# Performance work log

Measured on AMD Instinct MI355X. Metric: run time of the kernel, lower is better.

## Reference

```python
import jax, jax.numpy as jnp
import numpy as np

WIDE = 15
PAD = (WIDE - 1) // 2
FREQS = np.array([1., 2., 3., 4., 5., 6.], dtype=np.float32)  # wave_base_ml frequencies


def _lstm_dir(x, wih, whh, b):
    # x: [B,T,F]; wih: [4H,F]; whh: [4H,H]; b: [4H] (b_ih+b_hh fused)
    H = whh.shape[1]
    xg = jnp.einsum('btf,gf->btg', x, wih) + b  # precompute input projections
    def step(carry, xt):
        h, c = carry
        g = xt + h @ whh.T
        i, f, gg, o = jnp.split(g, 4, axis=-1)  # torch gate order i,f,g,o
        c = jax.nn.sigmoid(f) * c + jax.nn.sigmoid(i) * jnp.tanh(gg)
        h = jax.nn.sigmoid(o) * jnp.tanh(c)
        return (h, c), h
    h0 = jnp.zeros((x.shape[0], H), x.dtype)
    _, hs = jax.lax.scan(step, (h0, h0), jnp.swapaxes(xg, 0, 1))
    return jnp.swapaxes(hs, 0, 1)


def _bn(x, g, b, eps=1e-5):
    # training-mode BatchNorm1d over (N, L) per channel; x: [B,C,L]
    m = jnp.mean(x, axis=(0, 2), keepdims=True)
    v = jnp.var(x, axis=(0, 2), keepdims=True)
    return (x - m) * jax.lax.rsqrt(v + eps) * g[None, :, None] + b[None, :, None]


def _conv1d(x, w, b):
    y = jax.lax.conv_general_dilated(x, w, (1,), 'VALID', dimension_numbers=('NCH', 'OIH', 'NCH'))
    return y + b[None, :, None]


def _haar(x):
    s = 0.7071067811865476
    return (x[..., ::2] + x[..., 1::2]) * s, (x[..., ::2] - x[..., 1::2]) * s


def _forward(x, lstm_wif, lstm_whf, lstm_bf, lstm_wir, lstm_whr, lstm_br, base_w, base_b,
             g1, be1, g2, be2, g3, be3, g4, be4, g5, be5,
             w2, b2, w3, b3, w4, b4, w5, b5, fcw, fcb):
    xt = jnp.swapaxes(x, 1, 2)  # [B,T,F]
    fwd = _lstm_dir(xt, lstm_wif, lstm_whf, lstm_bf)
    bwd = _lstm_dir(xt[:, ::-1], lstm_wir, lstm_whr, lstm_br)[:, ::-1]
    X = jnp.swapaxes(jnp.concatenate([fwd, bwd], axis=-1), 1, 2)  # [B,C,T], C=2*dim
    B, C, T = X.shape
    Xp = jnp.pad(X, ((0, 0), (0, 0), (PAD, PAD)))
    # shared sliding windows [B,C,T,WIDE] used both for scale conv and Furi_conv
    Xwin = jnp.stack([Xp[..., k:k + T] for k in range(WIDE)], axis=-1)
    offs = (jnp.arange(WIDE, dtype=X.dtype) - PAD) / WIDE
    outs = []
    for ii in range(len(FREQS)):
        scales = jax.nn.relu(jnp.einsum('bctk,k->bct', Xwin, base_w[ii]) + base_b[ii])
        # per-position cosine Fourier basis generated from the learned scales
        bases = jnp.cos((2.0 * np.pi * FREQS[ii]) * scales[..., None] * offs)  # [B,C,T,WIDE]
        o = jnp.sum(Xwin * bases, axis=-1)  # position-dependent (dynamic) conv
        sqrs = jnp.sqrt((jnp.trunc(scales * WIDE) + 1.0) / (WIDE + 2) * 2.0)
        outs.append(o / sqrs)
    wave = jnp.stack(outs, axis=1).reshape(B, -1, T)  # [B, n_waves*C, T] (wave-major, matches torch cat+view)
    out = _bn(wave, g1, be1)
    out = _bn(jax.nn.relu(_conv1d(out, w2, b2)), g2, be2)
    out = _bn(jax.nn.relu(_conv1d(out, w3, b3)), g3, be3)
    out_back = out  # [B, V_dim, L3]
    out = _bn(jax.nn.relu(_conv1d(out, w4, b4)), g4, be4)  # [B,16,L3-2]
    # 4-level Haar DWT; 5 subbands upsampled to L3, averaged over channels
    a1, d1 = _haar(out_back); a2, d2 = _haar(a1); a3, d3 = _haar(a2); a4, d4 = _haar(a3)
    L3 = out_back.shape[-1]
    bands = [jnp.repeat(bb, L3 // bb.shape[-1], axis=-1) for bb in (a4, d4, d3, d2, d1)]
    dwt = jnp.stack([bb.mean(axis=1) for bb in bands], axis=1)  # [B,5,L3]
    odwt = _bn(jax.nn.relu(_conv1d(dwt, w5, b5)), g5, be5)  # [B,16,L3-2]
    out = jnp.concatenate([out, odwt], axis=-1)
    out = out.mean(axis=-1)  # AdaptiveAvgPool1d(1) + squeeze
    return out @ fcw.T + fcb


def setup_inputs() -> dict:
    key = jax.random.key(0)
    ks = iter(jax.random.split(key, 40))
    def p(shape, s=0.05):
        return jax.random.normal(next(ks), shape, jnp.float32) * s
    B, F, T, DIM, NW, Vd = 32, 64, 518, 64, 6, 32
    C = 2 * DIM
    return {
        'x': jax.random.normal(next(ks), (B, F, T), jnp.float32),
        'lstm_wif': p((4 * DIM, F)), 'lstm_whf': p((4 * DIM, DIM)), 'lstm_bf': p((4 * DIM,)),
        'lstm_wir': p((4 * DIM, F)), 'lstm_whr': p((4 * DIM, DIM)), 'lstm_br': p((4 * DIM,)),
        'base_w': p((NW, WIDE)), 'base_b': p((NW,)),
        'g1': jnp.ones((C * NW,)), 'be1': jnp.zeros((C * NW,)),
        'g2': jnp.ones((128,)), 'be2': jnp.zeros((128,)),
        'g3': jnp.ones((Vd,)), 'be3': jnp.zeros((Vd,)),
        'g4': jnp.ones((16,)), 'be4': jnp.zeros((16,)),
        'g5': jnp.ones((16,)), 'be5': jnp.zeros((16,)),
        'w2': p((128, C * NW, 3)), 'b2': p((128,)),
        'w3': p((Vd, 128, 5)), 'b3': p((Vd,)),
        'w4': p((16, Vd, 3)), 'b4': p((16,)),
        'w5': p((16, 5, 3)), 'b5': p((16,)),
        'fcw': p((10, 16)), 'fcb': p((10,)),
    }


def reference(x, lstm_wif, lstm_whf, lstm_bf, lstm_wir, lstm_whr, lstm_br, base_w, base_b,
              g1, be1, g2, be2, g3, be3, g4, be4, g5, be5,
              w2, b2, w3, b3, w4, b4, w5, b5, fcw, fcb):
    return _forward(x, lstm_wif, lstm_whf, lstm_bf, lstm_wir, lstm_whr, lstm_br, base_w, base_b,
                    g1, be1, g2, be2, g3, be3, g4, be4, g5, be5,
                    w2, b2, w3, b3, w4, b4, w5, b5, fcw, fcb)
```

## Files before the change

### kernel.cpp

```cpp
#include <hip/hip_runtime.h>
#include <math.h>

#define B_     32
#define F_     64
#define T_     518
#define HID    64
#define GATES  256
#define CCH    128
#define NWAVE  6
#define WCH    768
#define L2_    516
#define L3_    512
#define L4_    510

__device__ __forceinline__ float frcp(float x) { return __builtin_amdgcn_rcpf(x); }
__device__ __forceinline__ float fsigmoid(float x) { return frcp(1.f + __expf(-x)); }
__device__ __forceinline__ float ftanh(float x) { return 1.f - 2.f * frcp(1.f + __expf(2.f * x)); }

#define PIN8(a0,a1,a2,a3,a4,a5,a6,a7) \
    asm volatile("" : "+v"(a0), "+v"(a1), "+v"(a2), "+v"(a3), \
                      "+v"(a4), "+v"(a5), "+v"(a6), "+v"(a7))

__global__ void xg_kernel(const float* __restrict__ x,
                          const float* __restrict__ wif, const float* __restrict__ bf,
                          const float* __restrict__ wir, const float* __restrict__ br,
                          float* __restrict__ xg_f, float* __restrict__ xg_r,
                          float* __restrict__ stats) {
    if (blockIdx.x == 0 && blockIdx.y == 0) {
        for (int i = threadIdx.x; i < 2 * WCH; i += 256) stats[i] = 0.f;
    }
    const int tid = threadIdx.x;
    const int g   = tid;
    const int b   = blockIdx.y;
    const int t0  = blockIdx.x * 8;
    float4 wa[16], wb[16];
    const float4* w0 = (const float4*)(wif + g * F_);
    const float4* w1 = (const float4*)(wir + g * F_);
#pragma unroll
    for (int i = 0; i < 16; ++i) { wa[i] = w0[i]; wb[i] = w1[i]; }
    const float bfv = bf[g], brv = br[g];
    for (int tt = 0; tt < 8; ++tt) {
        const int t = t0 + tt;
        if (t >= T_) break;
        const float* xp = x + (size_t)b * F_ * T_ + t;
        float a0 = bfv, a1 = brv;
#pragma unroll
        for (int i = 0; i < 16; ++i) {
            float x0 = xp[(i * 4 + 0) * T_];
            float x1 = xp[(i * 4 + 1) * T_];
            float x2 = xp[(i * 4 + 2) * T_];
            float x3 = xp[(i * 4 + 3) * T_];
            a0 += wa[i].x * x0 + wa[i].y * x1 + wa[i].z * x2 + wa[i].w * x3;
            a1 += wb[i].x * x0 + wb[i].y * x1 + wb[i].z * x2 + wb[i].w * x3;
        }
        const size_t o = ((size_t)b * T_ + t) * GATES + tid;
        xg_f[o] = a0;
        xg_r[o] = a1;
    }
}

__global__ __attribute__((amdgpu_flat_work_group_size(256, 256),
                          amdgpu_waves_per_eu(1, 1)))
void lstm_kernel(
        const float* __restrict__ xgi_f, const float* __restrict__ xgi_r,
        const float* __restrict__ whf, const float* __restrict__ whr,
        float* __restrict__ X) {
    const int dir = blockIdx.x & 1;
    const int b   = blockIdx.x >> 1;
    const float* xg  = (dir ? xgi_r : xgi_f) + (size_t)b * T_ * GATES;
    const float* whh = dir ? whr : whf;
    const int tid = threadIdx.x;
    const int r   = tid & 63;
    const int w   = tid >> 6;

    float wreg[64];
    {
        const float4* p = (const float4*)(whh + (size_t)(w * HID + r) * HID);
#pragma unroll
        for (int i = 0; i < 16; ++i) {
            const float4 v = p[i];
            wreg[4 * i] = v.x; wreg[4 * i + 1] = v.y;
            wreg[4 * i + 2] = v.z; wreg[4 * i + 3] = v.w;
        }
    }
#pragma unroll
    for (int i = 0; i < 64; i += 8)
        PIN8(wreg[i], wreg[i + 1], wreg[i + 2], wreg[i + 3],
             wreg[i + 4], wreg[i + 5], wreg[i + 6], wreg[i + 7]);

    __shared__ __align__(16) float hs[4][HID];
    __shared__ float gbuf[2][4][HID];
    hs[w][r] = 0.f;
    float c = 0.f;
    float* Xrow = X + ((size_t)(b * CCH + dir * HID + r)) * T_;

    int t = dir ? (T_ - 1) : 0;
    const int step = dir ? -1 : 1;
    float q0 = xg[(size_t)t * GATES + tid];
    float q1 = xg[(size_t)(t + step) * GATES + tid];

    for (int s = 0; s < T_; ++s) {
        float a0 = q0, a1 = 0.f, a2 = 0.f, a3 = 0.f;
        const float4* h4p = (const float4*)hs[w];
#pragma unroll
        for (int i = 0; i < 16; ++i) {
            const float4 h4 = h4p[i];
            a0 = fmaf(wreg[4 * i], h4.x, a0);
            a1 = fmaf(wreg[4 * i + 1], h4.y, a1);
            a2 = fmaf(wreg[4 * i + 2], h4.z, a2);
            a3 = fmaf(wreg[4 * i + 3], h4.w, a3);
        }
        const int buf = s & 1;
        gbuf[buf][w][r] = (a0 + a1) + (a2 + a3);

        int tp = t + 2 * step;
        tp = tp < 0 ? 0 : (tp >= T_ ? T_ - 1 : tp);
        const float qn = xg[(size_t)tp * GATES + tid];

        asm volatile("s_waitcnt lgkmcnt(0)" ::: "memory");
        __builtin_amdgcn_s_barrier();

        const float gi = gbuf[buf][0][r];
        const float gf = gbuf[buf][1][r];
        const float gg = gbuf[buf][2][r];
        const float go = gbuf[buf][3][r];
        const float si = fsigmoid(gi);
        const float sf = fsigmoid(gf);
        const float so = fsigmoid(go);
        c = sf * c + si * ftanh(gg);
        const float h = so * ftanh(c);

        hs[w][r] = h;
        if (w == 0) Xrow[t] = h;
        q0 = q1; q1 = qn;
        t += step;
    }
}

__global__ void wave_kernel(const float* __restrict__ X,
                            const float* __restrict__ bw, const float* __restrict__ bb,
                            float* __restrict__ wave, float* __restrict__ stats) {
    const int b = blockIdx.z, c = blockIdx.y;
    const int t0 = blockIdx.x * 256;
    const int tid = threadIdx.x;
    __shared__ float xs[256 + 14];
    __shared__ float bws[NWAVE][16];
    __shared__ float bbs[NWAVE];
    __shared__ float red[4][12];
    const float* xrow = X + ((size_t)(b * CCH + c)) * T_;
    for (int i = tid; i < 270; i += 256) {
        int tt = t0 - 7 + i;
        xs[i] = (tt >= 0 && tt < T_) ? xrow[tt] : 0.f;
    }
    if (tid < NWAVE * 15) bws[tid / 15][tid % 15] = bw[tid];
    if (tid < NWAVE) bbs[tid] = bb[tid];
    __syncthreads();
    const int t = t0 + tid;
    float ls[NWAVE], lq[NWAVE];
#pragma unroll
    for (int ii = 0; ii < NWAVE; ++ii) { ls[ii] = 0.f; lq[ii] = 0.f; }
    if (t < T_) {
        float win[15];
#pragma unroll
        for (int k = 0; k < 15; ++k) win[k] = xs[tid + k];
        float e[8];
        e[0] = win[7];
#pragma unroll
        for (int m = 1; m < 8; ++m) e[m] = win[7 - m] + win[7 + m];
        const float c0 = 6.28318530717958647692f / 15.f;
#pragma unroll
        for (int ii = 0; ii < NWAVE; ++ii) {
            float sc = bbs[ii];
#pragma unroll
            for (int k = 0; k < 15; ++k) sc += win[k] * bws[ii][k];
            sc = fmaxf(sc, 0.f);
            const float phi = c0 * (float)(ii + 1) * sc;
            float o = e[0];
#pragma unroll
            for (int m = 1; m < 8; ++m) o += e[m] * __cosf(phi * (float)m);
            const float q = (truncf(sc * 15.f) + 1.f) * (2.f / 17.f);
            const float val = o * rsqrtf(q);
            wave[((size_t)(b * WCH + ii * CCH + c)) * T_ + t] = val;
            ls[ii] = val;
            lq[ii] = val * val;
        }
    }
#pragma unroll
    for (int off = 32; off > 0; off >>= 1) {
#pragma unroll
        for (int ii = 0; ii < NWAVE; ++ii) {
            ls[ii] += __shfl_down(ls[ii], off);
            lq[ii] += __shfl_down(lq[ii], off);
        }
    }
    if ((tid & 63) == 0) {
        const int w = tid >> 6;
#pragma unroll
        for (int ii = 0; ii < NWAVE; ++ii) { red[w][ii] = ls[ii]; red[w][6 + ii] = lq[ii]; }
    }
    __syncthreads();
    if (tid < 12) {
        const float a = red[0][tid] + red[1][tid] + red[2][tid] + red[3][tid];
        const int ii = tid % 6;
        const int ch = ii * CCH + c;
        atomicAdd(&stats[(tid >= 6 ? WCH : 0) + ch], a);
    }
}

__global__ void bn1_finalize_kernel(const float* __restrict__ stats,
                                    float* __restrict__ mean, float* __restrict__ rstd) {
    const int c = threadIdx.x;
    const float n = (float)(B_ * T_);
    const float m = stats[c] / n;
    const float v = stats[WCH + c] / n - m * m;
    mean[c] = m;
    rstd[c] = rsqrtf(v + 1e-5f);
}

__global__ void bn_stats_kernel(const float* __restrict__ x, int Bn, int C, int L,
                                float* __restrict__ mean, float* __restrict__ rstd) {
    const int c = blockIdx.x;
    const int tid = threadIdx.x;
    float s = 0.f, s2 = 0.f;
    for (int b = 0; b < Bn; ++b) {
        const float* row = x + ((size_t)b * C + c) * L;
        for (int l = tid; l < L; l += 256) { float v = row[l]; s += v; s2 += v * v; }
    }
#pragma unroll
    for (int off = 32; off > 0; off >>= 1) { s += __shfl_down(s, off); s2 += __shfl_down(s2, off); }
    __shared__ float ss[4], ss2[4];
    if ((tid & 63) == 0) { ss[tid >> 6] = s; ss2[tid >> 6] = s2; }
    __syncthreads();
    if (tid == 0) {
        float S = ss[0] + ss[1] + ss[2] + ss[3];
        float S2 = ss2[0] + ss2[1] + ss2[2] + ss2[3];
        float n = (float)(Bn * L);
        float m = S / n;
        float v = S2 / n - m * m;
        mean[c] = m;
        rstd[c] = rsqrtf(v + 1e-5f);
    }
}

__global__ void bnfold2_kernel(const float* __restrict__ w2, const float* __restrict__ b2,
                               const float* __restrict__ m1, const float* __restrict__ r1,
                               const float* __restrict__ g1, const float* __restrict__ be1,
                               float* __restrict__ w2t, float* __restrict__ b2t) {
    const int o = blockIdx.x, tid = threadIdx.x;
    float part = 0.f;
    for (int idx = tid; idx < WCH * 3; idx += 256) {
        const int c = idx / 3;
        const float sc = r1[c] * g1[c];
        const float sh = be1[c] - m1[c] * sc;
        const float wv = w2[(size_t)o * (WCH * 3) + idx];
        w2t[(size_t)idx * 128 + o] = wv * sc;
        part += wv * sh;
    }
#pragma unroll
    for (int off = 32; off > 0; off >>= 1) part += __shfl_down(part, off);
    __shared__ float red[4];
    if ((tid & 63) == 0) red[tid >> 6] = part;
    __syncthreads();
    if (tid == 0) b2t[o] = b2[o] + red[0] + red[1] + red[2] + red[3];
}

__global__ void bnfold3_kernel(const float* __restrict__ w3, const float* __restrict__ b3,
                               const float* __restrict__ m2, const float* __restrict__ r2,
                               const float* __restrict__ g2, const float* __restrict__ be2,
                               float* __restrict__ w3t, float* __restrict__ b3t) {
    const int o = blockIdx.x, tid = threadIdx.x;
    float part = 0.f;
    for (int idx = tid; idx < 128 * 5; idx += 256) {
        const int c = idx / 5;
        const float sc = r2[c] * g2[c];
        const float sh = be2[c] - m2[c] * sc;
        const float wv = w3[(size_t)o * 640 + idx];
        w3t[(size_t)idx * 32 + o] = wv * sc;
        part += wv * sh;
    }
#pragma unroll
    for (int off = 32; off > 0; off >>= 1) part += __shfl_down(part, off);
    __shared__ float red[4];
    if ((tid & 63) == 0) red[tid >> 6] = part;
    __syncthreads();
    if (tid == 0) b3t[o] = b3[o] + red[0] + red[1] + red[2] + red[3];
}

__global__ void bnfold4_kernel(const float* __restrict__ w4, const float* __restrict__ b4,
                               const float* __restrict__ m3, const float* __restrict__ r3,
                               const float* __restrict__ g3, const float* __restrict__ be3,
                               float* __restrict__ w4t, float* __restrict__ b4t,
                               float* __restrict__ bnp3) {
    const int o = blockIdx.x, tid = threadIdx.x;
    float part = 0.f;
    if (tid < 96) {
        const int c = tid / 3;
        const float sc = r3[c] * g3[c];
        const float sh = be3[c] - m3[c] * sc;
        const float wv = w4[(size_t)o * 96 + tid];
        w4t[(size_t)tid * 16 + o] = wv * sc;
        part = wv * sh;
    }
    if (o == 0 && tid >= 96) {
        const int ch = tid - 96;
        const float sc = r3[ch] * g3[ch];
        bnp3[ch] = sc;
        bnp3[32 + ch] = be3[ch] - m3[ch] * sc;
    }
#pragma unroll
    for (int off = 32; off > 0; off >>= 1) part += __shfl_down(part, off);
    __shared__ float red[2];
    if ((tid & 63) == 0) red[tid >> 6] = part;
    __syncthreads();
    if (tid == 0) b4t[o] = b4[o] + red[0] + red[1];
}

__global__ __launch_bounds__(256) void conv2_kernel(
        const float* __restrict__ in, const float* __restrict__ wt,
        const float* __restrict__ bt, float* __restrict__ out) {
    const int b  = blockIdx.x;
    const int t  = blockIdx.y * 256 + threadIdx.x;
    const int o0 = blockIdx.z * 16;
    if (t >= L2_) return;
    float acc[16];
#pragma unroll
    for (int j = 0; j < 16; ++j) acc[j] = bt[o0 + j];
    const float* inb = in + (size_t)b * WCH * T_ + t;
    for (int c = 0; c < WCH; ++c) {
        const float x0 = inb[c * T_], x1 = inb[c * T_ + 1], x2 = inb[c * T_ + 2];
        const float* wc = wt + (size_t)c * 384 + o0;
#pragma unroll
        for (int j = 0; j < 16; ++j)
            acc[j] = fmaf(x0, wc[j], fmaf(x1, wc[128 + j], fmaf(x2, wc[256 + j], acc[j])));
    }
    const size_t ob = ((size_t)b * 128 + o0) * L2_ + t;
#pragma unroll
    for (int j = 0; j < 16; ++j) out[ob + (size_t)j * L2_] = fmaxf(acc[j], 0.f);
}

__global__ __launch_bounds__(256) void conv3_kernel(
        const float* __restrict__ in, const float* __restrict__ wt,
        const float* __restrict__ bt, float* __restrict__ out) {
    const int b  = blockIdx.x;
    const int t  = blockIdx.y * 256 + threadIdx.x;
    const int o0 = blockIdx.z * 8;
    float acc[8];
#pragma unroll
    for (int j = 0; j < 8; ++j) acc[j] = bt[o0 + j];
    const float* inb = in + (size_t)b * 128 * L2_ + t;
    for (int c = 0; c < 128; ++c) {
        const float x0 = inb[c * L2_], x1 = inb[c * L2_ + 1], x2 = inb[c * L2_ + 2];
        const float x3 = inb[c * L2_ + 3], x4 = inb[c * L2_ + 4];
        const float* wc = wt + (size_t)c * 160 + o0;
#pragma unroll
        for (int j = 0; j < 8; ++j) {
            float a = fmaf(x0, wc[j], acc[j]);
            a = fmaf(x1, wc[32 + j], a);
            a = fmaf(x2, wc[64 + j], a);
            a = fmaf(x3, wc[96 + j], a);
            acc[j] = fmaf(x4, wc[128 + j], a);
        }
    }
    const size_t ob = ((size_t)b * 32 + o0) * L3_ + t;
#pragma unroll
    for (int j = 0; j < 8; ++j) out[ob + (size_t)j * L3_] = fmaxf(acc[j], 0.f);
}

__global__ __launch_bounds__(256) void conv4_kernel(
        const float* __restrict__ in, const float* __restrict__ wt,
        const float* __restrict__ bt, float* __restrict__ out) {
    const int b = blockIdx.x;
    const int t = blockIdx.y * 256 + threadIdx.x;
    if (t >= L4_) return;
    float acc[16];
#pragma unroll
    for (int j = 0; j < 16; ++j) acc[j] = bt[j];
    const float* inb = in + (size_t)b * 32 * L3_ + t;
    for (int c = 0; c < 32; ++c) {
        const float x0 = inb[c * L3_], x1 = inb[c * L3_ + 1], x2 = inb[c * L3_ + 2];
        const float* wc = wt + (size_t)c * 48;
#pragma unroll
        for (int j = 0; j < 16; ++j)
            acc[j] = fmaf(x0, wc[j], fmaf(x1, wc[16 + j], fmaf(x2, wc[32 + j], acc[j])));
    }
    const size_t ob = ((size_t)b * 16) * L4_ + t;
#pragma unroll
    for (int j = 0; j < 16; ++j) out[ob + (size_t)j * L4_] = fmaxf(acc[j], 0.f);
}

__global__ __launch_bounds__(512) void dwt_conv5_kernel(const float* __restrict__ y3,
                                                        const float* __restrict__ w5,
                                                        const float* __restrict__ b5,
                                                        const float* __restrict__ bnp3,
                                                        float* __restrict__ y5) {
    const int b = blockIdx.x, l = threadIdx.x;
    __shared__ float cm[L3_];
    __shared__ float bands[5][L3_];
    __shared__ float w5s[240];
    __shared__ float b5s[16];
    __shared__ float sc3s[32], sh3s[32];
    if (l < 240) w5s[l] = w5[l];
    if (l < 16) b5s[l] = b5[l];
    if (l >= 256 && l < 288) sc3s[l - 256] = bnp3[l - 256];
    if (l >= 288 && l < 320) sh3s[l - 288] = bnp3[32 + (l - 288)];
    __syncthreads();
    float s = 0.f, shs = 0.f;
    for (int ch = 0; ch < 32; ++ch) {
        s = fmaf(y3[((size_t)b * 32 + ch) * L3_ + l], sc3s[ch], s);
        shs += sh3s[ch];
    }
    cm[l] = (s + shs) * (1.f / 32.f);
    __syncthreads();
    const float s1 = 0.70710678118654752440f;
    const float s2c = 0.5f;
    const float s3 = 0.35355339059327378f;
    const float s4 = 0.25f;
    const int b16 = l & ~15, b8 = l & ~7, b4v = l & ~3, b2v = l & ~1;
    float sa = 0.f, sb = 0.f;
#pragma unroll
    for (int i = 0; i < 8; ++i) { sa += cm[b16 + i]; sb += cm[b16 + 8 + i]; }
    bands[0][l] = (sa + sb) * s4;
    bands[1][l] = (sa - sb) * s4;
    float ta = 0.f, tb = 0.f;
#pragma unroll
    for (int i = 0; i < 4; ++i) { ta += cm[b8 + i]; tb += cm[b8 + 4 + i]; }
    bands[2][l] = (ta - tb) * s3;
    bands[3][l] = (cm[b4v] + cm[b4v + 1] - cm[b4v + 2] - cm[b4v + 3]) * s2c;
    bands[4][l] = (cm[b2v] - cm[b2v + 1]) * s1;
    __syncthreads();
    if (l < L4_) {
        float in3[5][3];
#pragma unroll
        for (int c = 0; c < 5; ++c) {
            in3[c][0] = bands[c][l]; in3[c][1] = bands[c][l + 1]; in3[c][2] = bands[c][l + 2];
        }
#pragma unroll
        for (int o = 0; o < 16; ++o) {
            float acc = b5s[o];
#pragma unroll
            for (int c = 0; c < 5; ++c) {
                const float* wp = &w5s[(o * 5 + c) * 3];
                acc += in3[c][0] * wp[0] + in3[c][1] * wp[1] + in3[c][2] * wp[2];
            }
            y5[((size_t)b * 16 + o) * L4_ + l] = fmaxf(acc, 0.f);
        }
    }
}

__global__ __launch_bounds__(512) void tail_final_kernel(
        const float* __restrict__ y4, const float* __restrict__ y5,
        const float* __restrict__ g4, const float* __restrict__ be4,
        const float* __restrict__ g5, const float* __restrict__ be5,
        const float* __restrict__ fcw, const float* __restrict__ fcb,
        float* __restrict__ out) {
    const int p = threadIdx.x;
    const int b = p >> 4, ch = p & 15;
    const float2* p4 = (const float2*)(y4 + ((size_t)(b * 16 + ch)) * L4_);
    const float2* p5 = (const float2*)(y5 + ((size_t)(b * 16 + ch)) * L4_);
    float s4 = 0.f, q4 = 0.f, s5 = 0.f, q5 = 0.f;
    for (int i = 0; i < L4_ / 2; ++i) {
        float2 a = p4[i], bb2 = p5[i];
        s4 += a.x + a.y;  q4 += a.x * a.x + a.y * a.y;
        s5 += bb2.x + bb2.y; q5 += bb2.x * bb2.x + bb2.y * bb2.y;
    }
    __shared__ float S4[512], Q4[512], S5[512], Q5[512];
    __shared__ float M4[16], R4[16], M5[16], R5[16];
    __shared__ float pool[B_][16];
    S4[p] = s4; Q4[p] = q4; S5[p] = s5; Q5[p] = q5;
    __syncthreads();
    if (p < 16) {
        float ts = 0.f, tq = 0.f, us = 0.f, uq = 0.f;
        for (int bb = 0; bb < B_; ++bb) {
            ts += S4[bb * 16 + p]; tq += Q4[bb * 16 + p];
            us += S5[bb * 16 + p]; uq += Q5[bb * 16 + p];
        }
        const float n = (float)(B_ * L4_);
        float m = ts / n; M4[p] = m; R4[p] = rsqrtf(tq / n - m * m + 1e-5f);
        m = us / n;       M5[p] = m; R5[p] = rsqrtf(uq / n - m * m + 1e-5f);
    }
    __syncthreads();
    {
        const float mm4 = s4 / (float)L4_, mm5 = s5 / (float)L4_;
        const float v4 = (mm4 - M4[ch]) * R4[ch] * g4[ch] + be4[ch];
        const float v5 = (mm5 - M5[ch]) * R5[ch] * g5[ch] + be5[ch];
        pool[b][ch] = 0.5f * (v4 + v5);
    }
    __syncthreads();
    if (p < B_ * 10) {
        const int bb = p / 10, row = p - bb * 10;
        float a = fcb[row];
#pragma unroll
        for (int c = 0; c < 16; ++c) a += pool[bb][c] * fcw[row * 16 + c];
        out[bb * 10 + row] = a;
    }
}

extern "C" void kernel_launch(void* const* d_in, const int* in_sizes, int n_in,
                              void* d_out, int out_size, void* d_ws, size_t ws_size,
                              hipStream_t stream) {
    (void)in_sizes; (void)n_in; (void)out_size; (void)ws_size;
    const float* x   = (const float*)d_in[0];
    const float* wif = (const float*)d_in[1];
    const float* whf = (const float*)d_in[2];
    const float* bf  = (const float*)d_in[3];
    const float* wir = (const float*)d_in[4];
    const float* whr = (const float*)d_in[5];
    const float* br  = (const float*)d_in[6];
    const float* bw  = (const float*)d_in[7];
    const float* bb  = (const float*)d_in[8];
    const float* g1  = (const float*)d_in[9];  const float* be1 = (const float*)d_in[10];
    const float* g2  = (const float*)d_in[11]; const float* be2 = (const float*)d_in[12];
    const float* g3  = (const float*)d_in[13]; const float* be3 = (const float*)d_in[14];
    const float* g4  = (const float*)d_in[15]; const float* be4 = (const float*)d_in[16];
    const float* g5  = (const float*)d_in[17]; const float* be5 = (const float*)d_in[18];
    const float* w2  = (const float*)d_in[19]; const float* b2  = (const float*)d_in[20];
    const float* w3  = (const float*)d_in[21]; const float* b3  = (const float*)d_in[22];
    const float* w4  = (const float*)d_in[23]; const float* b4  = (const float*)d_in[24];
    const float* w5  = (const float*)d_in[25]; const float* b5  = (const float*)d_in[26];
    const float* fcw = (const float*)d_in[27]; const float* fcb = (const float*)d_in[28];
    float* out = (float*)d_out;
    float* ws  = (float*)d_ws;

    float* xg_f  = ws;
    float* xg_r  = ws + 4243456;
    float* wave  = ws;
    float* X     = ws + 12730368;
    float* y2    = ws + 14852096;
    float* y3    = ws + 16965632;
    float* y4    = ws + 17489920;
    float* y5    = ws + 17751040;
    float* stats = ws + 18012160;
    float* m1 = ws + 18013696; float* r1 = m1 + 768;
    float* m2 = r1 + 768;      float* r2 = m2 + 128;
    float* m3 = r2 + 128;      float* r3 = m3 + 32;
    float* w2t  = X;
    float* b2t  = X + 294912;
    float* w3t  = X + 295040;
    float* b3t  = X + 315520;
    float* w4t  = X + 315552;
    float* b4t  = X + 317088;
    float* bnp3 = X + 317104;

    xg_kernel<<<dim3(65, 32), 256, 0, stream>>>(x, wif, bf, wir, br, xg_f, xg_r, stats);
    lstm_kernel<<<dim3(64), 256, 0, stream>>>(xg_f, xg_r, whf, whr, X);
    wave_kernel<<<dim3(3, CCH, B_), 256, 0, stream>>>(X, bw, bb, wave, stats);
    bn1_finalize_kernel<<<dim3(1), 768, 0, stream>>>(stats, m1, r1);
    bnfold2_kernel<<<dim3(128), 256, 0, stream>>>(w2, b2, m1, r1, g1, be1, w2t, b2t);
    conv2_kernel<<<dim3(32, 3, 8), 256, 0, stream>>>(wave, w2t, b2t, y2);
    bn_stats_kernel<<<dim3(128), 256, 0, stream>>>(y2, B_, 128, L2_, m2, r2);
    bnfold3_kernel<<<dim3(32), 256, 0, stream>>>(w3, b3, m2, r2, g2, be2, w3t, b3t);
    conv3_kernel<<<dim3(32, 2, 4), 256, 0, stream>>>(y2, w3t, b3t, y3);
    bn_stats_kernel<<<dim3(32), 256, 0, stream>>>(y3, B_, 32, L3_, m3, r3);
    bnfold4_kernel<<<dim3(16), 128, 0, stream>>>(w4, b4, m3, r3, g3, be3, w4t, b4t, bnp3);
    conv4_kernel<<<dim3(32, 2), 256, 0, stream>>>(y3, w4t, b4t, y4);
    dwt_conv5_kernel<<<dim3(B_), 512, 0, stream>>>(y3, w5, b5, bnp3, y5);
    tail_final_kernel<<<dim3(1), 512, 0, stream>>>(y4, y5, g4, be4, g5, be5, fcw, fcb, out);
}
```

Before: 1.066 ms.

## Halve LSTM block to two gates per thread and fuse BN stats into convs

The LSTM recurrence now runs with 128 threads per block. Each thread holds two gate rows of the recurrent weights in registers and reads an interleaved float2 gate input, which the xg kernel now writes in that interleaved order. This cuts the per-step wave count and barrier cost but doubles the FMA chain per thread and raises register pressure. Separately, the standalone BN stats and finalize kernels are removed: conv2 and conv3 accumulate per-channel sum and sum-of-squares with wave shuffles and atomics, and the bnfold kernels derive scale and shift from those sums in shared memory. This drops several launches and full re-reads of y2 and y3, at the cost of atomics and a less numerically robust variance formula.

```diff
diff --git a/kernel.cpp b/kernel.cpp
--- a/kernel.cpp
+++ b/kernel.cpp
@@ -30,7 +30,10 @@
         for (int i = threadIdx.x; i < 2 * WCH; i += 256) stats[i] = 0.f;
     }
     const int tid = threadIdx.x;
-    const int g   = tid;
+    const int wv  = tid >> 7;
+    const int g2  = tid & 1;
+    const int r   = (tid >> 1) & 63;
+    const int g   = (2 * wv + g2) * 64 + r;
     const int b   = blockIdx.y;
     const int t0  = blockIdx.x * 8;
     float4 wa[16], wb[16];
@@ -59,7 +62,7 @@
     }
 }
 
-__global__ __attribute__((amdgpu_flat_work_group_size(256, 256),
+__global__ __attribute__((amdgpu_flat_work_group_size(128, 128),
                           amdgpu_waves_per_eu(1, 1)))
 void lstm_kernel(
         const float* __restrict__ xgi_f, const float* __restrict__ xgi_r,
@@ -73,22 +76,26 @@
     const int r   = tid & 63;
     const int w   = tid >> 6;
 
-    float wreg[64];
+    float wrA[64], wrB[64];
     {
-        const float4* p = (const float4*)(whh + (size_t)(w * HID + r) * HID);
+        const float4* pA = (const float4*)(whh + (size_t)((2 * w) * HID + r) * HID);
+        const float4* pB = (const float4*)(whh + (size_t)((2 * w + 1) * HID + r) * HID);
 #pragma unroll
         for (int i = 0; i < 16; ++i) {
-            const float4 v = p[i];
-            wreg[4 * i] = v.x; wreg[4 * i + 1] = v.y;
-            wreg[4 * i + 2] = v.z; wreg[4 * i + 3] = v.w;
-        }
-    }
-#pragma unroll
-    for (int i = 0; i < 64; i += 8)
-        PIN8(wreg[i], wreg[i + 1], wreg[i + 2], wreg[i + 3],
-             wreg[i + 4], wreg[i + 5], wreg[i + 6], wreg[i + 7]);
-
-    __shared__ __align__(16) float hs[4][HID];
+            const float4 va = pA[i], vb = pB[i];
+            wrA[4 * i] = va.x; wrA[4 * i + 1] = va.y; wrA[4 * i + 2] = va.z; wrA[4 * i + 3] = va.w;
+            wrB[4 * i] = vb.x; wrB[4 * i + 1] = vb.y; wrB[4 * i + 2] = vb.z; wrB[4 * i + 3] = vb.w;
+        }
+    }
+#pragma unroll
+    for (int i = 0; i < 64; i += 8) {
+        PIN8(wrA[i], wrA[i + 1], wrA[i + 2], wrA[i + 3],
+             wrA[i + 4], wrA[i + 5], wrA[i + 6], wrA[i + 7]);
+        PIN8(wrB[i], wrB[i + 1], wrB[i + 2], wrB[i + 3],
+             wrB[i + 4], wrB[i + 5], wrB[i + 6], wrB[i + 7]);
+    }
+
+    __shared__ __align__(16) float hs[2][HID];
     __shared__ float gbuf[2][4][HID];
     hs[w][r] = 0.f;
     float c = 0.f;
@@ -96,26 +103,33 @@
 
     int t = dir ? (T_ - 1) : 0;
     const int step = dir ? -1 : 1;
-    float q0 = xg[(size_t)t * GATES + tid];
-    float q1 = xg[(size_t)(t + step) * GATES + tid];
+    const float2* xg2 = (const float2*)xg;
+    float2 q0 = xg2[(size_t)t * 128 + w * 64 + r];
+    float2 q1 = xg2[(size_t)(t + step) * 128 + w * 64 + r];
 
     for (int s = 0; s < T_; ++s) {
-        float a0 = q0, a1 = 0.f, a2 = 0.f, a3 = 0.f;
+        float a0 = q0.x, a1 = 0.f, a2 = 0.f, a3 = 0.f;
+        float b0 = q0.y, b1 = 0.f, b2 = 0.f, b3 = 0.f;
         const float4* h4p = (const float4*)hs[w];
 #pragma unroll
         for (int i = 0; i < 16; ++i) {
             const float4 h4 = h4p[i];
-            a0 = fmaf(wreg[4 * i], h4.x, a0);
-            a1 = fmaf(wreg[4 * i + 1], h4.y, a1);
-            a2 = fmaf(wreg[4 * i + 2], h4.z, a2);
-            a3 = fmaf(wreg[4 * i + 3], h4.w, a3);
+            a0 = fmaf(wrA[4 * i], h4.x, a0);
+            a1 = fmaf(wrA[4 * i + 1], h4.y, a1);
+            a2 = fmaf(wrA[4 * i + 2], h4.z, a2);
+            a3 = fmaf(wrA[4 * i + 3], h4.w, a3);
+            b0 = fmaf(wrB[4 * i], h4.x, b0);
+            b1 = fmaf(wrB[4 * i + 1], h4.y, b1);
+            b2 = fmaf(wrB[4 * i + 2], h4.z, b2);
+            b3 = fmaf(wrB[4 * i + 3], h4.w, b3);
         }
         const int buf = s & 1;
-        gbuf[buf][w][r] = (a0 + a1) + (a2 + a3);
+        gbuf[buf][2 * w][r]     = (a0 + a1) + (a2 + a3);
+        gbuf[buf][2 * w + 1][r] = (b0 + b1) + (b2 + b3);
 
         int tp = t + 2 * step;
         tp = tp < 0 ? 0 : (tp >= T_ ? T_ - 1 : tp);
-        const float qn = xg[(size_t)tp * GATES + tid];
+        const float2 qn = xg2[(size_t)tp * 128 + w * 64 + r];
 
         asm volatile("s_waitcnt lgkmcnt(0)" ::: "memory");
         __builtin_amdgcn_s_barrier();
@@ -207,54 +221,29 @@
     }
 }
 
-__global__ void bn1_finalize_kernel(const float* __restrict__ stats,
-                                    float* __restrict__ mean, float* __restrict__ rstd) {
-    const int c = threadIdx.x;
+__global__ void bnfold2_kernel(const float* __restrict__ w2, const float* __restrict__ b2,
+                               const float* __restrict__ stats1,
+                               const float* __restrict__ g1, const float* __restrict__ be1,
+                               float* __restrict__ w2t, float* __restrict__ b2t,
+                               float* __restrict__ stats2) {
+    const int o = blockIdx.x, tid = threadIdx.x;
+    __shared__ float scs[WCH], shs[WCH];
     const float n = (float)(B_ * T_);
-    const float m = stats[c] / n;
-    const float v = stats[WCH + c] / n - m * m;
-    mean[c] = m;
-    rstd[c] = rsqrtf(v + 1e-5f);
-}
-
-__global__ void bn_stats_kernel(const float* __restrict__ x, int Bn, int C, int L,
-                                float* __restrict__ mean, float* __restrict__ rstd) {
-    const int c = blockIdx.x;
-    const int tid = threadIdx.x;
-    float s = 0.f, s2 = 0.f;
-    for (int b = 0; b < Bn; ++b) {
-        const float* row = x + ((size_t)b * C + c) * L;
-        for (int l = tid; l < L; l += 256) { float v = row[l]; s += v; s2 += v * v; }
-    }
-#pragma unroll
-    for (int off = 32; off > 0; off >>= 1) { s += __shfl_down(s, off); s2 += __shfl_down(s2, off); }
-    __shared__ float ss[4], ss2[4];
-    if ((tid & 63) == 0) { ss[tid >> 6] = s; ss2[tid >> 6] = s2; }
-    __syncthreads();
-    if (tid == 0) {
-        float S = ss[0] + ss[1] + ss[2] + ss[3];
-        float S2 = ss2[0] + ss2[1] + ss2[2] + ss2[3];
-        float n = (float)(Bn * L);
-        float m = S / n;
-        float v = S2 / n - m * m;
-        mean[c] = m;
-        rstd[c] = rsqrtf(v + 1e-5f);
-    }
-}
-
-__global__ void bnfold2_kernel(const float* __restrict__ w2, const float* __restrict__ b2,
-                               const float* __restrict__ m1, const float* __restrict__ r1,
-                               const float* __restrict__ g1, const float* __restrict__ be1,
-                               float* __restrict__ w2t, float* __restrict__ b2t) {
-    const int o = blockIdx.x, tid = threadIdx.x;
+    for (int ch = tid; ch < WCH; ch += 256) {
+        const float m = stats1[ch] / n;
+        const float v = stats1[WCH + ch] / n - m * m;
+        const float sc = rsqrtf(v + 1e-5f) * g1[ch];
+        scs[ch] = sc;
+        shs[ch] = be1[ch] - m * sc;
+    }
+    if (o == 0) { for (int i = tid; i < 256; i += 256) stats2[i] = 0.f; }
+    __syncthreads();
     float part = 0.f;
     for (int idx = tid; idx < WCH * 3; idx += 256) {
         const int c = idx / 3;
-        const float sc = r1[c] * g1[c];
-        const float sh = be1[c] - m1[c] * sc;
         const float wv = w2[(size_t)o * (WCH * 3) + idx];
-        w2t[(size_t)idx * 128 + o] = wv * sc;
-        part += wv * sh;
+        w2t[(size_t)idx * 128 + o] = wv * scs[c];
+        part += wv * shs[c];
     }
 #pragma unroll
     for (int off = 32; off > 0; off >>= 1) part += __shfl_down(part, off);
@@ -265,18 +254,28 @@
 }
 
 __global__ void bnfold3_kernel(const float* __restrict__ w3, const float* __restrict__ b3,
-                               const float* __restrict__ m2, const float* __restrict__ r2,
+                               const float* __restrict__ stats2,
                                const float* __restrict__ g2, const float* __restrict__ be2,
-                               float* __restrict__ w3t, float* __restrict__ b3t) {
+                               float* __restrict__ w3t, float* __restrict__ b3t,
+                               float* __restrict__ stats3) {
     const int o = blockIdx.x, tid = threadIdx.x;
+    __shared__ float scs[128], shs[128];
+    const float n = (float)(B_ * L2_);
+    if (tid < 128) {
+        const float m = stats2[tid] / n;
+        const float v = stats2[128 + tid] / n - m * m;
+        const float sc = rsqrtf(v + 1e-5f) * g2[tid];
+        scs[tid] = sc;
+        shs[tid] = be2[tid] - m * sc;
+    }
+    if (o == 0 && tid < 64) stats3[tid] = 0.f;
+    __syncthreads();
     float part = 0.f;
     for (int idx = tid; idx < 128 * 5; idx += 256) {
         const int c = idx / 5;
-        const float sc = r2[c] * g2[c];
-        const float sh = be2[c] - m2[c] * sc;
         const float wv = w3[(size_t)o * 640 + idx];
-        w3t[(size_t)idx * 32 + o] = wv * sc;
-        part += wv * sh;
+        w3t[(size_t)idx * 32 + o] = wv * scs[c];
+        part += wv * shs[c];
     }
 #pragma unroll
     for (int off = 32; off > 0; off >>= 1) part += __shfl_down(part, off);
@@ -287,26 +286,29 @@
 }
 
 __global__ void bnfold4_kernel(const float* __restrict__ w4, const float* __restrict__ b4,
-                               const float* __restrict__ m3, const float* __restrict__ r3,
+                               const float* __restrict__ stats3,
                                const float* __restrict__ g3, const float* __restrict__ be3,
                                float* __restrict__ w4t, float* __restrict__ b4t,
                                float* __restrict__ bnp3) {
     const int o = blockIdx.x, tid = threadIdx.x;
+    __shared__ float scs[32], shs[32];
+    const float n = (float)(B_ * L3_);
+    if (tid < 32) {
+        const float m = stats3[tid] / n;
+        const float v = stats3[32 + tid] / n - m * m;
+        const float sc = rsqrtf(v + 1e-5f) * g3[tid];
+        scs[tid] = sc;
+        shs[tid] = be3[tid] - m * sc;
+    }
+    __syncthreads();
     float part = 0.f;
     if (tid < 96) {
         const int c = tid / 3;
-        const float sc = r3[c] * g3[c];
-        const float sh = be3[c] - m3[c] * sc;
         const float wv = w4[(size_t)o * 96 + tid];
-        w4t[(size_t)tid * 16 + o] = wv * sc;
-        part = wv * sh;
-    }
-    if (o == 0 && tid >= 96) {
-        const int ch = tid - 96;
-        const float sc = r3[ch] * g3[ch];
-        bnp3[ch] = sc;
-        bnp3[32 + ch] = be3[ch] - m3[ch] * sc;
-    }
+        w4t[(size_t)tid * 16 + o] = wv * scs[c];
+        part = wv * shs[c];
+    }
+    if (o == 0 && tid < 32) { bnp3[tid] = scs[tid]; bnp3[32 + tid] = shs[tid]; }
 #pragma unroll
     for (int off = 32; off > 0; off >>= 1) part += __shfl_down(part, off);
     __shared__ float red[2];
@@ -317,33 +319,65 @@
 
 __global__ __launch_bounds__(256) void conv2_kernel(
         const float* __restrict__ in, const float* __restrict__ wt,
-        const float* __restrict__ bt, float* __restrict__ out) {
+        const float* __restrict__ bt, float* __restrict__ out,
+        float* __restrict__ stats2) {
     const int b  = blockIdx.x;
     const int t  = blockIdx.y * 256 + threadIdx.x;
     const int o0 = blockIdx.z * 16;
-    if (t >= L2_) return;
+    const int tid = threadIdx.x;
+    const bool valid = (t < L2_);
     float acc[16];
 #pragma unroll
     for (int j = 0; j < 16; ++j) acc[j] = bt[o0 + j];
-    const float* inb = in + (size_t)b * WCH * T_ + t;
-    for (int c = 0; c < WCH; ++c) {
-        const float x0 = inb[c * T_], x1 = inb[c * T_ + 1], x2 = inb[c * T_ + 2];
-        const float* wc = wt + (size_t)c * 384 + o0;
-#pragma unroll
-        for (int j = 0; j < 16; ++j)
-            acc[j] = fmaf(x0, wc[j], fmaf(x1, wc[128 + j], fmaf(x2, wc[256 + j], acc[j])));
-    }
-    const size_t ob = ((size_t)b * 128 + o0) * L2_ + t;
-#pragma unroll
-    for (int j = 0; j < 16; ++j) out[ob + (size_t)j * L2_] = fmaxf(acc[j], 0.f);
+    if (valid) {
+        const float* inb = in + (size_t)b * WCH * T_ + t;
+        for (int c = 0; c < WCH; ++c) {
+            const float x0 = inb[c * T_], x1 = inb[c * T_ + 1], x2 = inb[c * T_ + 2];
+            const float* wc = wt + (size_t)c * 384 + o0;
+#pragma unroll
+            for (int j = 0; j < 16; ++j)
+                acc[j] = fmaf(x0, wc[j], fmaf(x1, wc[128 + j], fmaf(x2, wc[256 + j], acc[j])));
+        }
+        const size_t ob = ((size_t)b * 128 + o0) * L2_ + t;
+#pragma unroll
+        for (int j = 0; j < 16; ++j) out[ob + (size_t)j * L2_] = fmaxf(acc[j], 0.f);
+    }
+    float ls[16], lq[16];
+#pragma unroll
+    for (int j = 0; j < 16; ++j) {
+        const float v = valid ? fmaxf(acc[j], 0.f) : 0.f;
+        ls[j] = v; lq[j] = v * v;
+    }
+#pragma unroll
+    for (int off = 32; off > 0; off >>= 1) {
+#pragma unroll
+        for (int j = 0; j < 16; ++j) {
+            ls[j] += __shfl_down(ls[j], off);
+            lq[j] += __shfl_down(lq[j], off);
+        }
+    }
+    __shared__ float red[4][32];
+    if ((tid & 63) == 0) {
+        const int w = tid >> 6;
+#pragma unroll
+        for (int j = 0; j < 16; ++j) { red[w][j] = ls[j]; red[w][16 + j] = lq[j]; }
+    }
+    __syncthreads();
+    if (tid < 32) {
+        const float a = red[0][tid] + red[1][tid] + red[2][tid] + red[3][tid];
+        const int ch = o0 + (tid & 15);
+        atomicAdd(&stats2[(tid >= 16 ? 128 : 0) + ch], a);
+    }
 }
 
 __global__ __launch_bounds__(256) void conv3_kernel(
         const float* __restrict__ in, const float* __restrict__ wt,
-        const float* __restrict__ bt, float* __restrict__ out) {
+        const float* __restrict__ bt, float* __restrict__ out,
+        float* __restrict__ stats3) {
     const int b  = blockIdx.x;
     const int t  = blockIdx.y * 256 + threadIdx.x;
     const int o0 = blockIdx.z * 8;
+    const int tid = threadIdx.x;
     float acc[8];
 #pragma unroll
     for (int j = 0; j < 8; ++j) acc[j] = bt[o0 + j];
@@ -362,8 +396,33 @@
         }
     }
     const size_t ob = ((size_t)b * 32 + o0) * L3_ + t;
-#pragma unroll
-    for (int j = 0; j < 8; ++j) out[ob + (size_t)j * L3_] = fmaxf(acc[j], 0.f);
+    float ls[8], lq[8];
+#pragma unroll
+    for (int j = 0; j < 8; ++j) {
+        const float v = fmaxf(acc[j], 0.f);
+        out[ob + (size_t)j * L3_] = v;
+        ls[j] = v; lq[j] = v * v;
+    }
+#pragma unroll
+    for (int off = 32; off > 0; off >>= 1) {
+#pragma unroll
+        for (int j = 0; j < 8; ++j) {
+            ls[j] += __shfl_down(ls[j], off);
+            lq[j] += __shfl_down(lq[j], off);
+        }
+    }
+    __shared__ float red[4][16];
+    if ((tid & 63) == 0) {
+        const int w = tid >> 6;
+#pragma unroll
+        for (int j = 0; j < 8; ++j) { red[w][j] = ls[j]; red[w][8 + j] = lq[j]; }
+    }
+    __syncthreads();
+    if (tid < 16) {
+        const float a = red[0][tid] + red[1][tid] + red[2][tid] + red[3][tid];
+        const int ch = o0 + (tid & 7);
+        atomicAdd(&stats3[(tid >= 8 ? 32 : 0) + ch], a);
+    }
 }
 
 __global__ __launch_bounds__(256) void conv4_kernel(
@@ -521,18 +580,17 @@
     float* out = (float*)d_out;
     float* ws  = (float*)d_ws;
 
-    float* xg_f  = ws;
-    float* xg_r  = ws + 4243456;
-    float* wave  = ws;
-    float* X     = ws + 12730368;
-    float* y2    = ws + 14852096;
-    float* y3    = ws + 16965632;
-    float* y4    = ws + 17489920;
-    float* y5    = ws + 17751040;
-    float* stats = ws + 18012160;
-    float* m1 = ws + 18013696; float* r1 = m1 + 768;
-    float* m2 = r1 + 768;      float* r2 = m2 + 128;
-    float* m3 = r2 + 128;      float* r3 = m3 + 32;
+    float* xg_f   = ws;
+    float* xg_r   = ws + 4243456;
+    float* wave   = ws;
+    float* X      = ws + 12730368;
+    float* y2     = ws + 14852096;
+    float* y3     = ws + 16965632;
+    float* y4     = ws + 17489920;
+    float* y5     = ws + 17751040;
+    float* stats1 = ws + 18012160;
+    float* stats2 = ws + 18013696;
+    float* stats3 = ws + 18013952;
     float* w2t  = X;
     float* b2t  = X + 294912;
     float* w3t  = X + 295040;
@@ -541,17 +599,14 @@
     float* b4t  = X + 317088;
     float* bnp3 = X + 317104;
 
-    xg_kernel<<<dim3(65, 32), 256, 0, stream>>>(x, wif, bf, wir, br, xg_f, xg_r, stats);
-    lstm_kernel<<<dim3(64), 256, 0, stream>>>(xg_f, xg_r, whf, whr, X);
-    wave_kernel<<<dim3(3, CCH, B_), 256, 0, stream>>>(X, bw, bb, wave, stats);
-    bn1_finalize_kernel<<<dim3(1), 768, 0, stream>>>(stats, m1, r1);
-    bnfold2_kernel<<<dim3(128), 256, 0, stream>>>(w2, b2, m1, r1, g1, be1, w2t, b2t);
-    conv2_kernel<<<dim3(32, 3, 8), 256, 0, stream>>>(wave, w2t, b2t, y2);
-    bn_stats_kernel<<<dim3(128), 256, 0, stream>>>(y2, B_, 128, L2_, m2, r2);
-    bnfold3_kernel<<<dim3(32), 256, 0, stream>>>(w3, b3, m2, r2, g2, be2, w3t, b3t);
-    conv3_kernel<<<dim3(32, 2, 4), 256, 0, stream>>>(y2, w3t, b3t, y3);
-    bn_stats_kernel<<<dim3(32), 256, 0, stream>>>(y3, B_, 32, L3_, m3, r3);
-    bnfold4_kernel<<<dim3(16), 128, 0, stream>>>(w4, b4, m3, r3, g3, be3, w4t, b4t, bnp3);
+    xg_kernel<<<dim3(65, 32), 256, 0, stream>>>(x, wif, bf, wir, br, xg_f, xg_r, stats1);
+    lstm_kernel<<<dim3(64), 128, 0, stream>>>(xg_f, xg_r, whf, whr, X);
+    wave_kernel<<<dim3(3, CCH, B_), 256, 0, stream>>>(X, bw, bb, wave, stats1);
+    bnfold2_kernel<<<dim3(128), 256, 0, stream>>>(w2, b2, stats1, g1, be1, w2t, b2t, stats2);
+    conv2_kernel<<<dim3(32, 3, 8), 256, 0, stream>>>(wave, w2t, b2t, y2, stats2);
+    bnfold3_kernel<<<dim3(32), 256, 0, stream>>>(w3, b3, stats2, g2, be2, w3t, b3t, stats3);
+    conv3_kernel<<<dim3(32, 2, 4), 256, 0, stream>>>(y2, w3t, b3t, y3, stats3);
+    bnfold4_kernel<<<dim3(16), 128, 0, stream>>>(w4, b4, stats3, g3, be3, w4t, b4t, bnp3);
     conv4_kernel<<<dim3(32, 2), 256, 0, stream>>>(y3, w4t, b4t, y4);
     dwt_conv5_kernel<<<dim3(B_), 512, 0, stream>>>(y3, w5, b5, bnp3, y5);
     tail_final_kernel<<<dim3(1), 512, 0, stream>>>(y4, y5, g4, be4, g5, be5, fcw, fcb, out);
```

Result: no change. 1.046 ms (-1.9%).
